# Kernel tuning notes

Measured on AMD Instinct MI355X. Metric: run time of the kernel, lower is better.

## Reference

```python
import jax, jax.numpy as jnp
import numpy as np

N_REVIEWS = 1_000_000
N_USERS = 100_000
N_ITEMS = 50_000
D = 64  # per-entity embedding dim; input_dim = 3*D = 192
D_OUT = 64


def setup_inputs() -> dict:
    key = jax.random.key(0)
    k1, k2, k3, k4, k5, k6, k7, k8 = jax.random.split(key, 8)
    review_vecs = jax.random.normal(k1, (N_REVIEWS, D), dtype=jnp.float32)
    user_vecs = jax.random.normal(k2, (N_USERS, D), dtype=jnp.float32)
    item_vecs = jax.random.normal(k3, (N_ITEMS, D), dtype=jnp.float32)
    W = jax.random.normal(k4, (3 * D, D_OUT), dtype=jnp.float32) * (1.0 / np.sqrt(3 * D))
    review_user_adj = jax.random.randint(k5, (N_REVIEWS,), 0, N_USERS, dtype=jnp.int32)
    review_item_adj = jax.random.randint(k6, (N_REVIEWS,), 0, N_ITEMS, dtype=jnp.int32)
    # tf.random_shuffle on the transposed gather shuffles the feature axis;
    # modeled as fixed permutations for determinism.
    perm_u = jax.random.permutation(k7, D).astype(jnp.int32)
    perm_i = jax.random.permutation(k8, D).astype(jnp.int32)
    return {
        "review_vecs": review_vecs,
        "user_vecs": user_vecs,
        "item_vecs": item_vecs,
        "W": W,
        "review_user_adj": review_user_adj,
        "review_item_adj": review_item_adj,
        "perm_u": perm_u,
        "perm_i": perm_i,
    }


def reference(review_vecs, user_vecs, item_vecs, W,
              review_user_adj, review_item_adj, perm_u, perm_i):
    # dropout = 0.0 -> identity
    ri = item_vecs[review_item_adj][:, perm_i]   # [N_reviews, D] gather + feature shuffle
    ru = user_vecs[review_user_adj][:, perm_u]   # [N_reviews, D]
    concat = jnp.concatenate([review_vecs, ru, ri], axis=1)  # [N_reviews, 3D]
    out = concat @ W                              # [N_reviews, D_OUT]
    return jax.nn.relu(out)
```

## Files before the change

### kernel.cpp

```cpp
#include <hip/hip_runtime.h>
#include <hip/hip_bf16.h>


#define DIMS 64
#define K3 192
#define MTILE 64
#define LDST 208

typedef float f32x4 __attribute__((ext_vector_type(4)));
typedef short s16x8 __attribute__((ext_vector_type(8)));
typedef __bf16 bf16x8 __attribute__((ext_vector_type(8)));

__device__ __forceinline__ short f2bf(float f) {
    union { float f; unsigned int u; } v; v.f = f;
    unsigned int u = v.u;
    u += 0x7fffu + ((u >> 16) & 1u);
    return (short)(u >> 16);
}

__global__ void prep_WT(const float* __restrict__ W,
                        const int* __restrict__ perm_u,
                        const int* __restrict__ perm_i,
                        short* __restrict__ WT) {
    const int t = threadIdx.x;
    #pragma unroll 4
    for (int i = 0; i < 48; ++i) {
        int e = t + i * 256;
        int k = e >> 6;
        int n = e & 63;
        float w = W[e];
        int dk;
        if (k < 64)       dk = k;
        else if (k < 128) dk = 64 + perm_u[k - 64];
        else              dk = 128 + perm_i[k - 128];
        WT[n * K3 + dk] = f2bf(w);
    }
}

__device__ __forceinline__ void stage16(const float* __restrict__ src, short* dst) {
    const float4* s4 = (const float4*)src;
    float4 a = s4[0], b = s4[1], c = s4[2], d = s4[3];
    s16x8 lo, hi;
    lo[0] = f2bf(a.x); lo[1] = f2bf(a.y); lo[2] = f2bf(a.z); lo[3] = f2bf(a.w);
    lo[4] = f2bf(b.x); lo[5] = f2bf(b.y); lo[6] = f2bf(b.z); lo[7] = f2bf(b.w);
    hi[0] = f2bf(c.x); hi[1] = f2bf(c.y); hi[2] = f2bf(c.z); hi[3] = f2bf(c.w);
    hi[4] = f2bf(d.x); hi[5] = f2bf(d.y); hi[6] = f2bf(d.z); hi[7] = f2bf(d.w);
    ((s16x8*)dst)[0] = lo;
    ((s16x8*)dst)[1] = hi;
}

__global__ __launch_bounds__(256) void concat_agg_kernel(
        const float* __restrict__ review,
        const float* __restrict__ user,
        const float* __restrict__ item,
        const int* __restrict__ uadj,
        const int* __restrict__ iadj,
        const short* __restrict__ WT,
        float* __restrict__ out,
        int n_reviews) {
    __shared__ short ldsX[MTILE * LDST];
    __shared__ short ldsW[DIMS * LDST];

    const int t = threadIdx.x;
    const int r0 = blockIdx.x * MTILE;

    #pragma unroll
    for (int i = 0; i < 6; ++i) {
        int c = t + i * 256;
        int n = c / 24;
        int k = (c - n * 24) * 8;
        s16x8 v = *(const s16x8*)(WT + c * 8);
        *(s16x8*)&ldsW[n * LDST + k] = v;
    }

    const int rloc = t >> 2;
    const int seg  = (t & 3) * 16;
    int row = r0 + rloc;
    if (row >= n_reviews) row = n_reviews - 1;

    stage16(review + (size_t)row * DIMS + seg, &ldsX[rloc * LDST + seg]);
    const int u  = uadj[row];
    stage16(user + (size_t)u * DIMS + seg, &ldsX[rloc * LDST + 64 + seg]);
    const int it = iadj[row];
    stage16(item + (size_t)it * DIMS + seg, &ldsX[rloc * LDST + 128 + seg]);

    __syncthreads();

    const int lane = t & 63;
    const int wv   = t >> 6;
    const int m    = lane & 15;
    const int q    = lane >> 4;

    const short* xa  = &ldsX[(wv * 16 + m) * LDST + q * 8];
    const short* wb0 = &ldsW[m * LDST + q * 8];

    f32x4 acc0 = {0.f,0.f,0.f,0.f}, acc1 = {0.f,0.f,0.f,0.f};
    f32x4 acc2 = {0.f,0.f,0.f,0.f}, acc3 = {0.f,0.f,0.f,0.f};

    #pragma unroll
    for (int ks = 0; ks < 6; ++ks) {
        bf16x8 a = __builtin_bit_cast(bf16x8, *(const s16x8*)(xa + ks * 32));
        bf16x8 b0 = __builtin_bit_cast(bf16x8, *(const s16x8*)(wb0 + 0 * 16 * LDST + ks * 32));
        bf16x8 b1 = __builtin_bit_cast(bf16x8, *(const s16x8*)(wb0 + 1 * 16 * LDST + ks * 32));
        bf16x8 b2 = __builtin_bit_cast(bf16x8, *(const s16x8*)(wb0 + 2 * 16 * LDST + ks * 32));
        bf16x8 b3 = __builtin_bit_cast(bf16x8, *(const s16x8*)(wb0 + 3 * 16 * LDST + ks * 32));
        acc0 = __builtin_amdgcn_mfma_f32_16x16x32_bf16(a, b0, acc0, 0, 0, 0);
        acc1 = __builtin_amdgcn_mfma_f32_16x16x32_bf16(a, b1, acc1, 0, 0, 0);
        acc2 = __builtin_amdgcn_mfma_f32_16x16x32_bf16(a, b2, acc2, 0, 0, 0);
        acc3 = __builtin_amdgcn_mfma_f32_16x16x32_bf16(a, b3, acc3, 0, 0, 0);
    }

    #pragma unroll
    for (int v = 0; v < 4; ++v) {
        const int rr = r0 + wv * 16 + q * 4 + v;
        if (rr < n_reviews) {
            float* orow = out + (size_t)rr * DIMS + m;
            orow[ 0] = fmaxf(acc0[v], 0.0f);
            orow[16] = fmaxf(acc1[v], 0.0f);
            orow[32] = fmaxf(acc2[v], 0.0f);
            orow[48] = fmaxf(acc3[v], 0.0f);
        }
    }
}

extern "C" void kernel_launch(void* const* d_in, const int* in_sizes, int n_in,
                              void* d_out, int out_size, void* d_ws, size_t ws_size,
                              hipStream_t stream) {
    (void)n_in; (void)out_size; (void)ws_size;
    const float* review = (const float*)d_in[0];
    const float* user   = (const float*)d_in[1];
    const float* item   = (const float*)d_in[2];
    const float* W      = (const float*)d_in[3];
    const int* uadj     = (const int*)d_in[4];
    const int* iadj     = (const int*)d_in[5];
    const int* perm_u   = (const int*)d_in[6];
    const int* perm_i   = (const int*)d_in[7];
    float* out = (float*)d_out;
    short* WT = (short*)d_ws;

    const int n_reviews = in_sizes[0] / DIMS;

    prep_WT<<<1, 256, 0, stream>>>(W, perm_u, perm_i, WT);

    const int grid = (n_reviews + MTILE - 1) / MTILE;
    concat_agg_kernel<<<grid, 256, 0, stream>>>(review, user, item, uadj, iadj,
                                                WT, out, n_reviews);
}
```

Measured before the change: 511.8 us.

## Load MFMA operands directly from global memory, dropping LDS staging

Each lane now loads its own A fragment (review, user and item rows) straight from global memory into registers and converts it to bf16, and reads the bf16 W^T fragments directly from global/L2. This removes the LDS tiles and the block barrier. It also adds nontemporal loads and stores for the streamed review input and output, a launch-bounds occupancy hint, and parallelizes the weight prep across 48 blocks. In exchange, every wave reloads W from cache instead of sharing it in LDS, and the per-lane loads are less coalesced (32-byte pieces per row).

```diff
diff --git a/kernel.cpp b/kernel.cpp
--- a/kernel.cpp
+++ b/kernel.cpp
@@ -4,8 +4,6 @@
 
 #define DIMS 64
 #define K3 192
-#define MTILE 64
-#define LDST 208
 
 typedef float f32x4 __attribute__((ext_vector_type(4)));
 typedef short s16x8 __attribute__((ext_vector_type(8)));
@@ -18,38 +16,29 @@
     return (short)(u >> 16);
 }
 
+__device__ __forceinline__ bf16x8 pack8(f32x4 x, f32x4 y) {
+    s16x8 r;
+    r[0] = f2bf(x[0]); r[1] = f2bf(x[1]); r[2] = f2bf(x[2]); r[3] = f2bf(x[3]);
+    r[4] = f2bf(y[0]); r[5] = f2bf(y[1]); r[6] = f2bf(y[2]); r[7] = f2bf(y[3]);
+    return __builtin_bit_cast(bf16x8, r);
+}
+
 __global__ void prep_WT(const float* __restrict__ W,
                         const int* __restrict__ perm_u,
                         const int* __restrict__ perm_i,
                         short* __restrict__ WT) {
-    const int t = threadIdx.x;
-    #pragma unroll 4
-    for (int i = 0; i < 48; ++i) {
-        int e = t + i * 256;
-        int k = e >> 6;
-        int n = e & 63;
-        float w = W[e];
-        int dk;
-        if (k < 64)       dk = k;
-        else if (k < 128) dk = 64 + perm_u[k - 64];
-        else              dk = 128 + perm_i[k - 128];
-        WT[n * K3 + dk] = f2bf(w);
-    }
+    const int e = blockIdx.x * 256 + threadIdx.x;
+    const int k = e >> 6;
+    const int n = e & 63;
+    const float w = W[e];
+    int dk;
+    if (k < 64)       dk = k;
+    else if (k < 128) dk = 64 + perm_u[k - 64];
+    else              dk = 128 + perm_i[k - 128];
+    WT[n * K3 + dk] = f2bf(w);
 }
 
-__device__ __forceinline__ void stage16(const float* __restrict__ src, short* dst) {
-    const float4* s4 = (const float4*)src;
-    float4 a = s4[0], b = s4[1], c = s4[2], d = s4[3];
-    s16x8 lo, hi;
-    lo[0] = f2bf(a.x); lo[1] = f2bf(a.y); lo[2] = f2bf(a.z); lo[3] = f2bf(a.w);
-    lo[4] = f2bf(b.x); lo[5] = f2bf(b.y); lo[6] = f2bf(b.z); lo[7] = f2bf(b.w);
-    hi[0] = f2bf(c.x); hi[1] = f2bf(c.y); hi[2] = f2bf(c.z); hi[3] = f2bf(c.w);
-    hi[4] = f2bf(d.x); hi[5] = f2bf(d.y); hi[6] = f2bf(d.z); hi[7] = f2bf(d.w);
-    ((s16x8*)dst)[0] = lo;
-    ((s16x8*)dst)[1] = hi;
-}
-
-__global__ __launch_bounds__(256) void concat_agg_kernel(
+__global__ __launch_bounds__(256, 6) void concat_agg_kernel(
         const float* __restrict__ review,
         const float* __restrict__ user,
         const float* __restrict__ item,
@@ -58,67 +47,71 @@
         const short* __restrict__ WT,
         float* __restrict__ out,
         int n_reviews) {
-    __shared__ short ldsX[MTILE * LDST];
-    __shared__ short ldsW[DIMS * LDST];
-
-    const int t = threadIdx.x;
-    const int r0 = blockIdx.x * MTILE;
-
-    #pragma unroll
-    for (int i = 0; i < 6; ++i) {
-        int c = t + i * 256;
-        int n = c / 24;
-        int k = (c - n * 24) * 8;
-        s16x8 v = *(const s16x8*)(WT + c * 8);
-        *(s16x8*)&ldsW[n * LDST + k] = v;
-    }
-
-    const int rloc = t >> 2;
-    const int seg  = (t & 3) * 16;
-    int row = r0 + rloc;
-    if (row >= n_reviews) row = n_reviews - 1;
-
-    stage16(review + (size_t)row * DIMS + seg, &ldsX[rloc * LDST + seg]);
-    const int u  = uadj[row];
-    stage16(user + (size_t)u * DIMS + seg, &ldsX[rloc * LDST + 64 + seg]);
-    const int it = iadj[row];
-    stage16(item + (size_t)it * DIMS + seg, &ldsX[rloc * LDST + 128 + seg]);
-
-    __syncthreads();
-
+    const int t    = threadIdx.x;
     const int lane = t & 63;
     const int wv   = t >> 6;
     const int m    = lane & 15;
     const int q    = lane >> 4;
 
-    const short* xa  = &ldsX[(wv * 16 + m) * LDST + q * 8];
-    const short* wb0 = &ldsW[m * LDST + q * 8];
+    const int tile = blockIdx.x * 4 + wv;
+    int row = tile * 16 + m;
+    if (row >= n_reviews) row = n_reviews - 1;
+
+    const int u  = uadj[row];
+    const int it = iadj[row];
+
+    const float* pr = review + (size_t)row * DIMS + q * 8;
+    const float* pu = user   + (size_t)u   * DIMS + q * 8;
+    const float* pi = item   + (size_t)it  * DIMS + q * 8;
+
+    f32x4 af0 = __builtin_nontemporal_load((const f32x4*)pr);
+    f32x4 af1 = __builtin_nontemporal_load((const f32x4*)pr + 1);
+    f32x4 af2 = __builtin_nontemporal_load((const f32x4*)(pr + 32));
+    f32x4 af3 = __builtin_nontemporal_load((const f32x4*)(pr + 32) + 1);
+    f32x4 af4 = ((const f32x4*)pu)[0];
+    f32x4 af5 = ((const f32x4*)pu)[1];
+    f32x4 af6 = ((const f32x4*)(pu + 32))[0];
+    f32x4 af7 = ((const f32x4*)(pu + 32))[1];
+    f32x4 af8 = ((const f32x4*)pi)[0];
+    f32x4 af9 = ((const f32x4*)pi)[1];
+    f32x4 afa = ((const f32x4*)(pi + 32))[0];
+    f32x4 afb = ((const f32x4*)(pi + 32))[1];
+
+    bf16x8 a[6];
+    a[0] = pack8(af0, af1);
+    a[1] = pack8(af2, af3);
+    a[2] = pack8(af4, af5);
+    a[3] = pack8(af6, af7);
+    a[4] = pack8(af8, af9);
+    a[5] = pack8(afa, afb);
+
+    const short* wbase = WT + m * K3 + q * 8;
 
     f32x4 acc0 = {0.f,0.f,0.f,0.f}, acc1 = {0.f,0.f,0.f,0.f};
     f32x4 acc2 = {0.f,0.f,0.f,0.f}, acc3 = {0.f,0.f,0.f,0.f};
 
     #pragma unroll
     for (int ks = 0; ks < 6; ++ks) {
-        bf16x8 a = __builtin_bit_cast(bf16x8, *(const s16x8*)(xa + ks * 32));
-        bf16x8 b0 = __builtin_bit_cast(bf16x8, *(const s16x8*)(wb0 + 0 * 16 * LDST + ks * 32));
-        bf16x8 b1 = __builtin_bit_cast(bf16x8, *(const s16x8*)(wb0 + 1 * 16 * LDST + ks * 32));
-        bf16x8 b2 = __builtin_bit_cast(bf16x8, *(const s16x8*)(wb0 + 2 * 16 * LDST + ks * 32));
-        bf16x8 b3 = __builtin_bit_cast(bf16x8, *(const s16x8*)(wb0 + 3 * 16 * LDST + ks * 32));
-        acc0 = __builtin_amdgcn_mfma_f32_16x16x32_bf16(a, b0, acc0, 0, 0, 0);
-        acc1 = __builtin_amdgcn_mfma_f32_16x16x32_bf16(a, b1, acc1, 0, 0, 0);
-        acc2 = __builtin_amdgcn_mfma_f32_16x16x32_bf16(a, b2, acc2, 0, 0, 0);
-        acc3 = __builtin_amdgcn_mfma_f32_16x16x32_bf16(a, b3, acc3, 0, 0, 0);
+        bf16x8 b0 = __builtin_bit_cast(bf16x8, *(const s16x8*)(wbase + 0 * 16 * K3 + ks * 32));
+        bf16x8 b1 = __builtin_bit_cast(bf16x8, *(const s16x8*)(wbase + 1 * 16 * K3 + ks * 32));
+        bf16x8 b2 = __builtin_bit_cast(bf16x8, *(const s16x8*)(wbase + 2 * 16 * K3 + ks * 32));
+        bf16x8 b3 = __builtin_bit_cast(bf16x8, *(const s16x8*)(wbase + 3 * 16 * K3 + ks * 32));
+        acc0 = __builtin_amdgcn_mfma_f32_16x16x32_bf16(a[ks], b0, acc0, 0, 0, 0);
+        acc1 = __builtin_amdgcn_mfma_f32_16x16x32_bf16(a[ks], b1, acc1, 0, 0, 0);
+        acc2 = __builtin_amdgcn_mfma_f32_16x16x32_bf16(a[ks], b2, acc2, 0, 0, 0);
+        acc3 = __builtin_amdgcn_mfma_f32_16x16x32_bf16(a[ks], b3, acc3, 0, 0, 0);
     }
 
+    const int rbase = tile * 16 + q * 4;
     #pragma unroll
     for (int v = 0; v < 4; ++v) {
-        const int rr = r0 + wv * 16 + q * 4 + v;
+        const int rr = rbase + v;
         if (rr < n_reviews) {
             float* orow = out + (size_t)rr * DIMS + m;
-            orow[ 0] = fmaxf(acc0[v], 0.0f);
-            orow[16] = fmaxf(acc1[v], 0.0f);
-            orow[32] = fmaxf(acc2[v], 0.0f);
-            orow[48] = fmaxf(acc3[v], 0.0f);
+            __builtin_nontemporal_store(fmaxf(acc0[v], 0.0f), orow +  0);
+            __builtin_nontemporal_store(fmaxf(acc1[v], 0.0f), orow + 16);
+            __builtin_nontemporal_store(fmaxf(acc2[v], 0.0f), orow + 32);
+            __builtin_nontemporal_store(fmaxf(acc3[v], 0.0f), orow + 48);
         }
     }
 }
@@ -140,9 +133,9 @@
 
     const int n_reviews = in_sizes[0] / DIMS;
 
-    prep_WT<<<1, 256, 0, stream>>>(W, perm_u, perm_i, WT);
+    prep_WT<<<48, 256, 0, stream>>>(W, perm_u, perm_i, WT);
 
-    const int grid = (n_reviews + MTILE - 1) / MTILE;
+    const int grid = (n_reviews + 63) / 64;
     concat_agg_kernel<<<grid, 256, 0, stream>>>(review, user, item, uadj, iadj,
                                                 WT, out, n_reviews);
 }
```

New measurement: 642.2 us. 25.5% more time.
